# Kernel tuning notes

Measured on AMD Instinct MI355X. Metric: run time of the kernel, lower is better.

## Reference

```python
import jax, jax.numpy as jnp
import numpy as np

# MLS-MPM constants (init_kwargs)
N_GRID = 128
DT = 2e-4
DX = 1.0 / N_GRID
INV_DX = float(N_GRID)
P_VOL = (DX * 0.5) ** 3
P_RHO = 1000.0
P_MASS = P_VOL * P_RHO
GRAVITY = 9.8
BOUND = 3
N_PART = 500_000

# 27 neighbor offsets for quadratic B-spline stencil
_OFFS = np.stack(np.meshgrid(np.arange(3), np.arange(3), np.arange(3), indexing='ij'), -1).reshape(27, 3)


def setup_inputs() -> dict:
    key = jax.random.key(0)
    k1, k2, k3, k4, k5 = jax.random.split(key, 5)
    # particles strictly inside the domain, away from boundary cells
    x = 0.2 + 0.6 * jax.random.uniform(k1, (N_PART, 3), dtype=jnp.float32)
    v = 0.1 * jax.random.normal(k2, (N_PART, 3), dtype=jnp.float32)
    C = 0.1 * jax.random.normal(k3, (N_PART, 3, 3), dtype=jnp.float32)
    F = jnp.eye(3, dtype=jnp.float32) + 0.01 * jax.random.normal(k4, (N_PART, 3, 3), dtype=jnp.float32)
    stress = 1e2 * jax.random.normal(k5, (N_PART, 3, 3), dtype=jnp.float32)
    return {"x": x, "v": v, "C": C, "F": F, "stress": stress}


def _mpm_step(x, v, C, F, stress):
    dtype = x.dtype
    base = jnp.floor(x * INV_DX - 0.5).astype(jnp.int32)          # [N,3]
    fx = x * INV_DX - base.astype(dtype)                          # [N,3] in [0.5, 1.5)
    # quadratic B-spline weights per node offset (0,1,2) per axis: [N,3off,3ax]
    w = jnp.stack([0.5 * (1.5 - fx) ** 2,
                   0.75 - (fx - 1.0) ** 2,
                   0.5 * (fx - 0.5) ** 2], axis=1)
    offs = jnp.asarray(_OFFS, dtype=jnp.int32)                    # [27,3]
    weight = w[:, offs[:, 0], 0] * w[:, offs[:, 1], 1] * w[:, offs[:, 2], 2]  # [N,27]
    dpos = (offs[None].astype(dtype) - fx[:, None, :]) * DX       # [N,27,3] world units

    # P2G scatter: momentum (3) + mass (1) per grid node
    affine = (-DT * P_VOL * 4.0 * INV_DX * INV_DX) * stress + P_MASS * C   # [N,3,3]
    mv = P_MASS * v[:, None, :] + jnp.einsum('nij,nkj->nki', affine, dpos) # [N,27,3]
    vals = jnp.concatenate([weight[..., None] * mv,
                            (weight * P_MASS)[..., None]], axis=-1)        # [N,27,4]
    node = jnp.clip(base[:, None, :] + offs[None], 0, N_GRID - 1)          # [N,27,3]
    flat = (node[..., 0] * N_GRID + node[..., 1]) * N_GRID + node[..., 2]  # [N,27]
    grid = jnp.zeros((N_GRID ** 3, 4), dtype).at[flat.reshape(-1)].add(vals.reshape(-1, 4))

    # grid update: normalize momentum, gravity, sticky boundary
    gm = grid[:, 3:4]
    occ = gm[:, 0] > 0
    gv = jnp.where(gm > 0, grid[:, :3] / jnp.maximum(gm, 1e-10), 0.0)
    gv = gv.at[:, 1].add(jnp.where(occ, jnp.asarray(-DT * GRAVITY, dtype), 0.0))
    gv3 = gv.reshape(N_GRID, N_GRID, N_GRID, 3)
    idx = jnp.arange(N_GRID)
    for axis in range(3):  # fixed 3-axis loop (not a data loop)
        shp = [1, 1, 1]; shp[axis] = N_GRID
        lo = (idx < BOUND).reshape(shp)
        hi = (idx >= N_GRID - BOUND).reshape(shp)
        comp = gv3[..., axis]
        comp = jnp.where(lo & (comp < 0), 0.0, comp)
        comp = jnp.where(hi & (comp > 0), 0.0, comp)
        gv3 = gv3.at[..., axis].set(comp)
    gvf = gv3.reshape(-1, 3)

    # G2P gather
    gvp = gvf[flat]                                               # [N,27,3]
    v_next = jnp.einsum('nk,nkd->nd', weight, gvp)
    C_next = (4.0 * INV_DX * INV_DX) * jnp.einsum('nk,nki,nkj->nij', weight, gvp, dpos)
    x_next = x + DT * v_next
    F_next = jnp.einsum('nij,njk->nik', jnp.eye(3, dtype=dtype) + DT * C_next, F)
    return x_next, v_next, C_next, F_next


def reference(x, v, C, F, stress):
    return _mpm_step(x, v, C, F, stress)
```

## Files before the change

kernel.cpp:

```cpp
#include <hip/hip_runtime.h>
#include <limits.h>

#define N_GRID 128
#define N_GRID3 (N_GRID * N_GRID * N_GRID)

constexpr int   N_PART   = 500000;
constexpr float DT       = 0.0002f;
constexpr float DX       = 1.0f / 128.0f;
constexpr float INV_DX   = 128.0f;
constexpr float P_MASS   = 5.9604644775390625e-05f;
constexpr float AFF_COEF = -7.8125e-07f;
constexpr float GRAVITY  = 9.8f;
constexpr int   BOUND    = 3;
constexpr float C_SCALE  = 65536.0f;
constexpr int   ZQ       = 2;

__global__ __launch_bounds__(256) void k_count(const float* __restrict__ x,
                                               int* __restrict__ cnt,
                                               int* __restrict__ blkMin,
                                               int* __restrict__ blkMax) {
  __shared__ int lmin[12], lmax[12];
  int n = blockIdx.x * 256 + threadIdx.x;
  int bx = INT_MAX, by = INT_MAX, bz = INT_MAX;
  int mx = -1, my = -1, mz = -1;
  if (n < N_PART) {
    bx = min(max((int)floorf(x[n * 3 + 0] * INV_DX - 0.5f), 0), N_GRID - 1);
    by = min(max((int)floorf(x[n * 3 + 1] * INV_DX - 0.5f), 0), N_GRID - 1);
    bz = min(max((int)floorf(x[n * 3 + 2] * INV_DX - 0.5f), 0), N_GRID - 1);
    int c = (bx << 14) | (by << 7) | bz;
    atomicAdd(&cnt[c], 1);
    mx = bx; my = by; mz = bz;
  }
#pragma unroll
  for (int d = 32; d > 0; d >>= 1) {
    bx = min(bx, __shfl_xor(bx, d));
    by = min(by, __shfl_xor(by, d));
    bz = min(bz, __shfl_xor(bz, d));
    mx = max(mx, __shfl_xor(mx, d));
    my = max(my, __shfl_xor(my, d));
    mz = max(mz, __shfl_xor(mz, d));
  }
  int lane = threadIdx.x & 63, wid = threadIdx.x >> 6;
  if (lane == 0) {
    lmin[wid * 3 + 0] = bx; lmin[wid * 3 + 1] = by; lmin[wid * 3 + 2] = bz;
    lmax[wid * 3 + 0] = mx; lmax[wid * 3 + 1] = my; lmax[wid * 3 + 2] = mz;
  }
  __syncthreads();
  if (threadIdx.x == 0) {
    int b = blockIdx.x;
#pragma unroll
    for (int a = 0; a < 3; ++a) {
      blkMin[b * 3 + a] = min(min(lmin[a], lmin[3 + a]), min(lmin[6 + a], lmin[9 + a]));
      blkMax[b * 3 + a] = max(max(lmax[a], lmax[3 + a]), max(lmax[6 + a], lmax[9 + a]));
    }
  }
}

__global__ __launch_bounds__(256) void k_scan1(const int* __restrict__ cnt,
                                               int* __restrict__ blkSum) {
  __shared__ int ws[4];
  int tid = threadIdx.x, lane = tid & 63, wid = tid >> 6;
  int4 v = ((const int4*)cnt)[blockIdx.x * 256 + tid];
  int s = v.x + v.y + v.z + v.w;
  for (int d = 32; d > 0; d >>= 1) s += __shfl_down(s, d);
  if (lane == 0) ws[wid] = s;
  __syncthreads();
  if (tid == 0) blkSum[blockIdx.x] = ws[0] + ws[1] + ws[2] + ws[3];
}

__global__ __launch_bounds__(256) void k_scan2(const int* __restrict__ blkSum,
                                               int* __restrict__ blkOff,
                                               int* __restrict__ start,
                                               const int* __restrict__ blkMin,
                                               const int* __restrict__ blkMax,
                                               int nblkP,
                                               int* __restrict__ bbox) {
  __shared__ int wsum[4];
  __shared__ int rmin[12], rmax[12];
  int tid = threadIdx.x, lane = tid & 63, wid = tid >> 6;

  int base = tid * 8;
  int s[8], tot = 0;
#pragma unroll
  for (int j = 0; j < 8; ++j) { s[j] = blkSum[base + j]; tot += s[j]; }
  int incl = tot;
  for (int d = 1; d < 64; d <<= 1) {
    int t = __shfl_up(incl, d);
    if (lane >= d) incl += t;
  }
  if (lane == 63) wsum[wid] = incl;
  __syncthreads();
  int woff = 0;
  for (int w = 0; w < wid; ++w) woff += wsum[w];
  int run = woff + incl - tot;
#pragma unroll
  for (int j = 0; j < 8; ++j) { blkOff[base + j] = run; run += s[j]; }
  if (tid == 255) start[N_GRID3] = run;

  int bx = INT_MAX, by = INT_MAX, bz = INT_MAX;
  int mx = -1, my = -1, mz = -1;
  for (int j = tid; j < nblkP; j += 256) {
    bx = min(bx, blkMin[j * 3 + 0]);
    by = min(by, blkMin[j * 3 + 1]);
    bz = min(bz, blkMin[j * 3 + 2]);
    mx = max(mx, blkMax[j * 3 + 0]);
    my = max(my, blkMax[j * 3 + 1]);
    mz = max(mz, blkMax[j * 3 + 2]);
  }
#pragma unroll
  for (int d = 32; d > 0; d >>= 1) {
    bx = min(bx, __shfl_xor(bx, d));
    by = min(by, __shfl_xor(by, d));
    bz = min(bz, __shfl_xor(bz, d));
    mx = max(mx, __shfl_xor(mx, d));
    my = max(my, __shfl_xor(my, d));
    mz = max(mz, __shfl_xor(mz, d));
  }
  if (lane == 0) {
    rmin[wid * 3 + 0] = bx; rmin[wid * 3 + 1] = by; rmin[wid * 3 + 2] = bz;
    rmax[wid * 3 + 0] = mx; rmax[wid * 3 + 1] = my; rmax[wid * 3 + 2] = mz;
  }
  __syncthreads();
  if (tid == 0) {
#pragma unroll
    for (int a = 0; a < 3; ++a) {
      bbox[a]     = min(min(rmin[a], rmin[3 + a]), min(rmin[6 + a], rmin[9 + a]));
      bbox[3 + a] = max(max(rmax[a], rmax[3 + a]), max(rmax[6 + a], rmax[9 + a]));
    }
  }
}

__global__ __launch_bounds__(256) void k_scan3(int* __restrict__ cnt,
                                               const int* __restrict__ blkOff,
                                               int* __restrict__ start) {
  __shared__ int wsum[4];
  int tid = threadIdx.x, lane = tid & 63, wid = tid >> 6;
  int b = blockIdx.x;
  int4 v = ((const int4*)cnt)[b * 256 + tid];
  int s = v.x + v.y + v.z + v.w;
  int incl = s;
  for (int d = 1; d < 64; d <<= 1) {
    int t = __shfl_up(incl, d);
    if (lane >= d) incl += t;
  }
  if (lane == 63) wsum[wid] = incl;
  __syncthreads();
  int woff = blkOff[b];
  for (int w = 0; w < wid; ++w) woff += wsum[w];
  int run = woff + incl - s;
  int i0 = (b * 256 + tid) * 4;
  int r0 = run, r1 = r0 + v.x, r2 = r1 + v.y, r3 = r2 + v.z;
  start[i0 + 0] = r0; start[i0 + 1] = r1; start[i0 + 2] = r2; start[i0 + 3] = r3;
  cnt[i0 + 0] = r0; cnt[i0 + 1] = r1; cnt[i0 + 2] = r2; cnt[i0 + 3] = r3;
}

__global__ __launch_bounds__(256) void k_reorder(
    const float* __restrict__ x, const float* __restrict__ v,
    const float* __restrict__ C, const float* __restrict__ S,
    int* __restrict__ cursor, float4* __restrict__ posO,
    float4* __restrict__ aux) {
  int n = blockIdx.x * 256 + threadIdx.x;
  if (n >= N_PART) return;

  float px = x[n * 3 + 0], py = x[n * 3 + 1], pz = x[n * 3 + 2];
  int bx = min(max((int)floorf(px * INV_DX - 0.5f), 0), N_GRID - 1);
  int by = min(max((int)floorf(py * INV_DX - 0.5f), 0), N_GRID - 1);
  int bz = min(max((int)floorf(pz * INV_DX - 0.5f), 0), N_GRID - 1);
  int c = (bx << 14) | (by << 7) | bz;
  int pos = atomicAdd(&cursor[c], 1);

  float mvx = P_MASS * v[n * 3 + 0];
  float mvy = P_MASS * v[n * 3 + 1];
  float mvz = P_MASS * v[n * 3 + 2];
  float aff[9];
#pragma unroll
  for (int k = 0; k < 9; ++k)
    aff[k] = AFF_COEF * S[n * 9 + k] + P_MASS * C[n * 9 + k];

  posO[pos] = make_float4(px, py, pz, __int_as_float(n));
  float4* dst = aux + (size_t)pos * 3;
  dst[0] = make_float4(mvx, mvy, mvz, aff[0]);
  dst[1] = make_float4(aff[1], aff[2], aff[3], aff[4]);
  dst[2] = make_float4(aff[5], aff[6], aff[7], aff[8]);
}

__device__ __forceinline__ float wq(int o, float f) {
  if (o == 0) return 0.5f * (1.5f - f) * (1.5f - f);
  if (o == 1) return 0.75f - (f - 1.0f) * (f - 1.0f);
  return 0.5f * (f - 0.5f) * (f - 0.5f);
}

__global__ __launch_bounds__(256) void mpm_p2g(
    const int* __restrict__ start, const float4* __restrict__ posO,
    const float4* __restrict__ aux, const int* __restrict__ bbox,
    float* __restrict__ grid ) {
  int bx0 = bbox[0], by0 = bbox[1], bz0c = bbox[2];
  int nxd = bbox[3] - bx0 + 3;
  int nyd = bbox[4] - by0 + 3;
  int nzd = bbox[5] - bz0c + 3;
  int dimzq = (nzd + ZQ - 1) / ZQ;
  int vol = nxd * nyd * dimzq;
  int nact = (vol + 255) >> 8;

  int bid = blockIdx.x;
  if (bid >= nact) return;
  int q = nact >> 3, r = nact & 7;
  int xcd = bid & 7, sub = bid >> 3;
  int wgid = (xcd < r ? xcd * (q + 1) : r * (q + 1) + (xcd - r) * q) + sub;

  int t = wgid * 256 + (int)threadIdx.x;
  if (t >= vol) return;
  int izq = t % dimzq;
  int rr = t / dimzq;
  int iy = rr % nyd;
  int ix = rr / nyd;
  int nx = bx0 + ix, ny = by0 + iy, nz0 = bz0c + izq * ZQ;
  if (nx > N_GRID - 1 || ny > N_GRID - 1) return;
  int zb0 = nz0 - 2;
  bool zint = (zb0 >= 0) && (zb0 + ZQ + 2 <= N_GRID);

  float accx[ZQ], accy[ZQ], accz[ZQ], accm[ZQ];
#pragma unroll
  for (int k = 0; k < ZQ; ++k) { accx[k] = 0.f; accy[k] = 0.f; accz[k] = 0.f; accm[k] = 0.f; }
  int gotmask = 0;

#pragma unroll
  for (int dy = -2; dy <= 0; ++dy) {
    int cy = ny + dy;
    if (cy < 0) continue;
#pragma unroll
    for (int dx = -2; dx <= 0; ++dx) {
      int cx = nx + dx;
      if (cx < 0) continue;
      const int ox = -dx, oy = -dy;
      int rowb = (cx << 14) | (cy << 7);

      int S[ZQ + 3];
      if (zint) {
#pragma unroll
        for (int j = 0; j < ZQ + 3; ++j) S[j] = start[rowb + zb0 + j];
      } else {
#pragma unroll
        for (int j = 0; j < ZQ + 3; ++j)
          S[j] = start[rowb + min(max(zb0 + j, 0), N_GRID)];
      }
#pragma unroll
      for (int k = 0; k < ZQ; ++k)
        gotmask |= (S[k + 3] > S[k]) ? (1 << k) : 0;

      for (int i = S[0]; i < S[ZQ + 2]; ++i) {
        float4 q0 = posO[i];
        const float4* ap = aux + (size_t)i * 3;
        float4 A0 = ap[0], A1 = ap[1], A2 = ap[2];

        float fx = q0.x * INV_DX - (float)cx;
        float fy = q0.y * INV_DX - (float)cy;
        float gz = q0.z * INV_DX;
        float bzf = floorf(gz - 0.5f);
        float fz = gz - bzf;
        int oz0 = nz0 - (int)bzf;

        float wxy = wq(ox, fx) * wq(oy, fy);
        float dpx = ((float)ox - fx) * DX;
        float dpy = ((float)oy - fy) * DX;
        float wz0 = 0.5f * (1.5f - fz) * (1.5f - fz);
        float wz1 = 0.75f - (fz - 1.0f) * (fz - 1.0f);
        float wz2 = 0.5f * (fz - 0.5f) * (fz - 0.5f);

        float sx = A0.x + A0.w * dpx + A1.x * dpy;
        float sy = A0.y + A1.z * dpx + A1.w * dpy;
        float sz = A0.z + A2.y * dpx + A2.z * dpy;
        float wm = wxy * P_MASS;

#pragma unroll
        for (int k = 0; k < ZQ; ++k) {
          int oz = oz0 + k;
          if (oz < 0 || oz > 2) continue;
          float wzz = (oz == 0) ? wz0 : ((oz == 1) ? wz1 : wz2);
          float w = wxy * wzz;
          float dpz = ((float)oz - fz) * DX;
          accx[k] += w * (sx + A1.y * dpz);
          accy[k] += w * (sy + A2.x * dpz);
          accz[k] += w * (sz + A2.w * dpz);
          accm[k] += wzz * wm;
        }
      }
    }
  }

  if (!gotmask) return;

  float4* g4 = (float4*)grid;
#pragma unroll
  for (int k = 0; k < ZQ; ++k) {
    int nz = nz0 + k;
    if (!((gotmask >> k) & 1) || nz > N_GRID - 1) continue;
    float m = accm[k];
    float ovx = 0.0f, ovy = 0.0f, ovz = 0.0f;
    if (m > 0.0f) {
      float inv = 1.0f / fmaxf(m, 1e-10f);
      ovx = accx[k] * inv;
      ovy = accy[k] * inv;
      ovz = accz[k] * inv;
      ovy -= DT * GRAVITY;
    }
    if (nx < BOUND && ovx < 0.0f) ovx = 0.0f;
    if (nx >= N_GRID - BOUND && ovx > 0.0f) ovx = 0.0f;
    if (ny < BOUND && ovy < 0.0f) ovy = 0.0f;
    if (ny >= N_GRID - BOUND && ovy > 0.0f) ovy = 0.0f;
    if (nz < BOUND && ovz < 0.0f) ovz = 0.0f;
    if (nz >= N_GRID - BOUND && ovz > 0.0f) ovz = 0.0f;
    g4[(nx << 14) | (ny << 7) | nz] = make_float4(ovx, ovy, ovz, m);
  }
}

__global__ __launch_bounds__(256) void mpm_g2p(
    const float4* __restrict__ posO, const float* __restrict__ F,
    const float* __restrict__ grid,
    float* __restrict__ out_x, float* __restrict__ out_v,
    float* __restrict__ out_C, float* __restrict__ out_F) {
  int i = blockIdx.x * blockDim.x + threadIdx.x;
  if (i >= N_PART) return;

  float4 q0 = posO[i];
  int n = __float_as_int(q0.w);

  float px = q0.x, py = q0.y, pz = q0.z;
  float gx = px * INV_DX, gy = py * INV_DX, gz = pz * INV_DX;
  int bx = (int)floorf(gx - 0.5f);
  int by = (int)floorf(gy - 0.5f);
  int bz = (int)floorf(gz - 0.5f);
  float fx = gx - (float)bx, fy = gy - (float)by, fz = gz - (float)bz;

  float wx[3], wy[3], wz[3];
  wx[0] = 0.5f * (1.5f - fx) * (1.5f - fx);
  wx[1] = 0.75f - (fx - 1.0f) * (fx - 1.0f);
  wx[2] = 0.5f * (fx - 0.5f) * (fx - 0.5f);
  wy[0] = 0.5f * (1.5f - fy) * (1.5f - fy);
  wy[1] = 0.75f - (fy - 1.0f) * (fy - 1.0f);
  wy[2] = 0.5f * (fy - 0.5f) * (fy - 0.5f);
  wz[0] = 0.5f * (1.5f - fz) * (1.5f - fz);
  wz[1] = 0.75f - (fz - 1.0f) * (fz - 1.0f);
  wz[2] = 0.5f * (fz - 0.5f) * (fz - 0.5f);

  float vnx = 0.0f, vny = 0.0f, vnz = 0.0f;
  float Cn[9];
#pragma unroll
  for (int k = 0; k < 9; ++k) Cn[k] = 0.0f;

  const float4* g4 = (const float4*)grid;
  bool interior = (bx >= 0) & (by >= 0) & (bz >= 0) &
                  (bx + 2 < N_GRID) & (by + 2 < N_GRID) & (bz + 2 < N_GRID);

  if (interior) {
    int flat0 = (bx << 14) | (by << 7) | bz;
#pragma unroll
    for (int a = 0; a < 3; ++a) {
#pragma unroll
      for (int bb = 0; bb < 3; ++bb) {
#pragma unroll
        for (int c = 0; c < 3; ++c) {
          float weight = wx[a] * wy[bb] * wz[c];
          float dpx = ((float)a - fx) * DX;
          float dpy = ((float)bb - fy) * DX;
          float dpz = ((float)c - fz) * DX;
          float4 g = g4[flat0 + (a << 14) + (bb << 7) + c];
          vnx += weight * g.x;
          vny += weight * g.y;
          vnz += weight * g.z;
          Cn[0] += weight * g.x * dpx;
          Cn[1] += weight * g.x * dpy;
          Cn[2] += weight * g.x * dpz;
          Cn[3] += weight * g.y * dpx;
          Cn[4] += weight * g.y * dpy;
          Cn[5] += weight * g.y * dpz;
          Cn[6] += weight * g.z * dpx;
          Cn[7] += weight * g.z * dpy;
          Cn[8] += weight * g.z * dpz;
        }
      }
    }
  } else {
#pragma unroll
    for (int a = 0; a < 3; ++a) {
#pragma unroll
      for (int bb = 0; bb < 3; ++bb) {
#pragma unroll
        for (int c = 0; c < 3; ++c) {
          float weight = wx[a] * wy[bb] * wz[c];
          float dpx = ((float)a - fx) * DX;
          float dpy = ((float)bb - fy) * DX;
          float dpz = ((float)c - fz) * DX;
          int nxg = min(max(bx + a, 0), N_GRID - 1);
          int nyg = min(max(by + bb, 0), N_GRID - 1);
          int nzg = min(max(bz + c, 0), N_GRID - 1);
          float4 g = g4[(nxg << 14) | (nyg << 7) | nzg];
          vnx += weight * g.x;
          vny += weight * g.y;
          vnz += weight * g.z;
          Cn[0] += weight * g.x * dpx;
          Cn[1] += weight * g.x * dpy;
          Cn[2] += weight * g.x * dpz;
          Cn[3] += weight * g.y * dpx;
          Cn[4] += weight * g.y * dpy;
          Cn[5] += weight * g.y * dpz;
          Cn[6] += weight * g.z * dpx;
          Cn[7] += weight * g.z * dpy;
          Cn[8] += weight * g.z * dpz;
        }
      }
    }
  }

#pragma unroll
  for (int k = 0; k < 9; ++k) Cn[k] *= C_SCALE;

  out_x[n * 3 + 0] = px + DT * vnx;
  out_x[n * 3 + 1] = py + DT * vny;
  out_x[n * 3 + 2] = pz + DT * vnz;
  out_v[n * 3 + 0] = vnx;
  out_v[n * 3 + 1] = vny;
  out_v[n * 3 + 2] = vnz;

  float A[9];
#pragma unroll
  for (int k = 0; k < 9; ++k) A[k] = DT * Cn[k];
  A[0] += 1.0f; A[4] += 1.0f; A[8] += 1.0f;

  float Fl[9];
#pragma unroll
  for (int k = 0; k < 9; ++k) Fl[k] = F[n * 9 + k];

#pragma unroll
  for (int r = 0; r < 3; ++r) {
#pragma unroll
    for (int k = 0; k < 3; ++k) {
      float s = A[r * 3 + 0] * Fl[0 * 3 + k] +
                A[r * 3 + 1] * Fl[1 * 3 + k] +
                A[r * 3 + 2] * Fl[2 * 3 + k];
      out_F[n * 9 + r * 3 + k] = s;
    }
  }

#pragma unroll
  for (int k = 0; k < 9; ++k) out_C[n * 9 + k] = Cn[k];
}

extern "C" void kernel_launch(void* const* d_in, const int* in_sizes, int n_in,
                              void* d_out, int out_size, void* d_ws, size_t ws_size,
                              hipStream_t stream) {
  const float* x      = (const float*)d_in[0];
  const float* v      = (const float*)d_in[1];
  const float* C      = (const float*)d_in[2];
  const float* F      = (const float*)d_in[3];
  const float* stress = (const float*)d_in[4];

  float* out = (float*)d_out;
  char*  ws  = (char*)d_ws;

  const size_t GRID_BYTES  = (size_t)N_GRID3 * 4 * sizeof(float);
  const size_t POSO_BYTES  = (size_t)N_PART * sizeof(float4);
  const size_t AUX_BYTES   = (size_t)N_PART * 3 * sizeof(float4);
  const size_t CNT_BYTES   = (size_t)N_GRID3 * sizeof(int);
  const size_t START_BYTES = ((size_t)N_GRID3 + 1) * sizeof(int);

  int pblocks = (N_PART + 255) / 256;

  float*  grid   = (float*)ws;
  float4* posO   = (float4*)(ws + GRID_BYTES);
  float4* aux    = (float4*)(ws + GRID_BYTES + POSO_BYTES);
  int*    cnt    = (int*)(ws + GRID_BYTES + POSO_BYTES + AUX_BYTES);
  int*    startp = (int*)(ws + GRID_BYTES + POSO_BYTES + AUX_BYTES + CNT_BYTES);
  int*    blkSum = (int*)(ws + GRID_BYTES + POSO_BYTES + AUX_BYTES + CNT_BYTES + START_BYTES);
  int*    blkOff = blkSum + 2048;
  int*    blkMin = blkOff + 2048;
  int*    blkMax = blkMin + pblocks * 3;
  int*    bbox   = blkMax + pblocks * 3;

  hipMemsetAsync(cnt, 0, CNT_BYTES, stream);

  k_count<<<pblocks, 256, 0, stream>>>(x, cnt, blkMin, blkMax);
  k_scan1<<<2048, 256, 0, stream>>>(cnt, blkSum);
  k_scan2<<<1, 256, 0, stream>>>(blkSum, blkOff, startp, blkMin, blkMax, pblocks, bbox);
  k_scan3<<<2048, 256, 0, stream>>>(cnt, blkOff, startp);
  k_reorder<<<pblocks, 256, 0, stream>>>(x, v, C, stress, cnt, posO, aux);

  mpm_p2g<<<(N_GRID3 / ZQ + 255) / 256, 256, 0, stream>>>(startp, posO, aux, bbox, grid);

  float* out_x = out;
  float* out_v = out + (size_t)N_PART * 3;
  float* out_C = out + (size_t)N_PART * 6;
  float* out_F = out + (size_t)N_PART * 6 + (size_t)N_PART * 9;
  mpm_g2p<<<pblocks, 256, 0, stream>>>(posO, F, grid, out_x, out_v, out_C, out_F);
}
```

Before: 204.9 us.

## Tile P2G gather into 8x8x4 node bricks with particles staged in LDS

The per-thread gather P2G, where each thread read particles from global memory for its two z-nodes, becomes a brick-based kernel. Each 256-thread workgroup owns an 8x8x4 node brick and computes the cell column prefix sums of its halo region. It cooperatively copies all contributing particles (position plus affine data) into shared memory, and each thread then accumulates its node from LDS, cutting repeated global and L2 reads of the same particle by neighbouring nodes. Bricks whose halo holds more than 896 particles fall back to the direct global-memory path. The shared-memory footprint (~58KB) limits occupancy, and the per-particle binary search and extra barriers add overhead.

```diff
diff --git a/kernel.cpp b/kernel.cpp
--- a/kernel.cpp
+++ b/kernel.cpp
@@ -13,7 +13,13 @@
 constexpr float GRAVITY  = 9.8f;
 constexpr int   BOUND    = 3;
 constexpr float C_SCALE  = 65536.0f;
-constexpr int   ZQ       = 2;
+
+constexpr int BBX = 8, BBY = 8, BBZ = 4;
+constexpr int RX = BBX + 2, RY = BBY + 2;
+constexpr int NCOL = RX * RY;
+constexpr int RZB = BBZ + 3;
+constexpr int CAP = 896;
+constexpr int MAX_BRICKS = 17 * 17 * 33;
 
 __global__ __launch_bounds__(256) void k_count(const float* __restrict__ x,
                                                int* __restrict__ cnt,
@@ -194,124 +200,206 @@
     const int* __restrict__ start, const float4* __restrict__ posO,
     const float4* __restrict__ aux, const int* __restrict__ bbox,
     float* __restrict__ grid ) {
+  __shared__ float4 ldsPos[CAP];
+  __shared__ float4 ldsA0[CAP];
+  __shared__ float4 ldsA1[CAP];
+  __shared__ float4 ldsA2[CAP];
+  __shared__ int    ldsBnd[NCOL * RZB];
+  __shared__ int    colSrc[NCOL];
+  __shared__ int    colPre[NCOL + 1];
+  __shared__ int    s_w0tot;
+
   int bx0 = bbox[0], by0 = bbox[1], bz0c = bbox[2];
-  int nxd = bbox[3] - bx0 + 3;
-  int nyd = bbox[4] - by0 + 3;
-  int nzd = bbox[5] - bz0c + 3;
-  int dimzq = (nzd + ZQ - 1) / ZQ;
-  int vol = nxd * nyd * dimzq;
-  int nact = (vol + 255) >> 8;
-
+  int nxd = bbox[3] - bx0 + 3, nyd = bbox[4] - by0 + 3, nzd = bbox[5] - bz0c + 3;
+  int nbx = (nxd + BBX - 1) / BBX;
+  int nby = (nyd + BBY - 1) / BBY;
+  int nbz = (nzd + BBZ - 1) / BBZ;
+  int nact = nbx * nby * nbz;
   int bid = blockIdx.x;
   if (bid >= nact) return;
   int q = nact >> 3, r = nact & 7;
   int xcd = bid & 7, sub = bid >> 3;
-  int wgid = (xcd < r ? xcd * (q + 1) : r * (q + 1) + (xcd - r) * q) + sub;
-
-  int t = wgid * 256 + (int)threadIdx.x;
-  if (t >= vol) return;
-  int izq = t % dimzq;
-  int rr = t / dimzq;
-  int iy = rr % nyd;
-  int ix = rr / nyd;
-  int nx = bx0 + ix, ny = by0 + iy, nz0 = bz0c + izq * ZQ;
-  if (nx > N_GRID - 1 || ny > N_GRID - 1) return;
-  int zb0 = nz0 - 2;
-  bool zint = (zb0 >= 0) && (zb0 + ZQ + 2 <= N_GRID);
-
-  float accx[ZQ], accy[ZQ], accz[ZQ], accm[ZQ];
-#pragma unroll
-  for (int k = 0; k < ZQ; ++k) { accx[k] = 0.f; accy[k] = 0.f; accz[k] = 0.f; accm[k] = 0.f; }
-  int gotmask = 0;
-
-#pragma unroll
-  for (int dy = -2; dy <= 0; ++dy) {
-    int cy = ny + dy;
-    if (cy < 0) continue;
-#pragma unroll
-    for (int dx = -2; dx <= 0; ++dx) {
-      int cx = nx + dx;
-      if (cx < 0) continue;
-      const int ox = -dx, oy = -dy;
-      int rowb = (cx << 14) | (cy << 7);
-
-      int S[ZQ + 3];
-      if (zint) {
-#pragma unroll
-        for (int j = 0; j < ZQ + 3; ++j) S[j] = start[rowb + zb0 + j];
-      } else {
-#pragma unroll
-        for (int j = 0; j < ZQ + 3; ++j)
-          S[j] = start[rowb + min(max(zb0 + j, 0), N_GRID)];
+  int wg = (xcd < r ? xcd * (q + 1) : r * (q + 1) + (xcd - r) * q) + sub;
+  int bzi = wg % nbz; int tt = wg / nbz; int byi = tt % nby; int bxi = tt / nby;
+  int ox = bx0 + bxi * BBX, oy = by0 + byi * BBY, oz = bz0c + bzi * BBZ;
+
+  int tid = threadIdx.x;
+
+  int cnt_t = 0;
+  if (tid < NCOL) {
+    int rcx = tid / RY, rcy = tid % RY;
+    int sx = ox - 2 + rcx, sy = oy - 2 + rcy;
+    int b[RZB];
+    if (sx >= 0 && sx < N_GRID && sy >= 0 && sy < N_GRID) {
+      int rowb = (sx << 14) | (sy << 7);
+      int zl0 = oz - 2;
+#pragma unroll
+      for (int j = 0; j < RZB; ++j)
+        b[j] = start[rowb + min(max(zl0 + j, 0), N_GRID)];
+    } else {
+#pragma unroll
+      for (int j = 0; j < RZB; ++j) b[j] = 0;
+    }
+    colSrc[tid] = b[0];
+#pragma unroll
+    for (int j = 0; j < RZB; ++j) ldsBnd[tid * RZB + j] = b[j] - b[0];
+    cnt_t = b[RZB - 1] - b[0];
+  }
+  int excl = 0;
+  if (tid < 128) {
+    int lane = tid & 63;
+    int incl = cnt_t;
+#pragma unroll
+    for (int d = 1; d < 64; d <<= 1) {
+      int tv = __shfl_up(incl, d);
+      if (lane >= d) incl += tv;
+    }
+    excl = incl - cnt_t;
+    if (tid == 63) s_w0tot = incl;
+  }
+  __syncthreads();
+  if (tid < 128) {
+    int off = (tid >= 64) ? s_w0tot : 0;
+    if (tid < NCOL) colPre[tid] = excl + off;
+    if (tid == 127) colPre[NCOL] = excl + off;
+  }
+  __syncthreads();
+  int T = colPre[NCOL];
+  if (T == 0) return;
+  bool overflow = (T > CAP);
+
+  if (!overflow) {
+    if (tid < NCOL) {
+      int p0 = colPre[tid];
+#pragma unroll
+      for (int j = 0; j < RZB; ++j) ldsBnd[tid * RZB + j] += p0;
+    }
+    __syncthreads();
+    for (int p = tid; p < T; p += 256) {
+      int lo = 0, hi = NCOL;
+      while (hi - lo > 1) {
+        int mid = (lo + hi) >> 1;
+        if (colPre[mid] <= p) lo = mid; else hi = mid;
       }
-#pragma unroll
-      for (int k = 0; k < ZQ; ++k)
-        gotmask |= (S[k + 3] > S[k]) ? (1 << k) : 0;
-
-      for (int i = S[0]; i < S[ZQ + 2]; ++i) {
-        float4 q0 = posO[i];
-        const float4* ap = aux + (size_t)i * 3;
-        float4 A0 = ap[0], A1 = ap[1], A2 = ap[2];
-
-        float fx = q0.x * INV_DX - (float)cx;
-        float fy = q0.y * INV_DX - (float)cy;
-        float gz = q0.z * INV_DX;
-        float bzf = floorf(gz - 0.5f);
-        float fz = gz - bzf;
-        int oz0 = nz0 - (int)bzf;
-
-        float wxy = wq(ox, fx) * wq(oy, fy);
-        float dpx = ((float)ox - fx) * DX;
-        float dpy = ((float)oy - fy) * DX;
-        float wz0 = 0.5f * (1.5f - fz) * (1.5f - fz);
-        float wz1 = 0.75f - (fz - 1.0f) * (fz - 1.0f);
-        float wz2 = 0.5f * (fz - 0.5f) * (fz - 0.5f);
-
-        float sx = A0.x + A0.w * dpx + A1.x * dpy;
-        float sy = A0.y + A1.z * dpx + A1.w * dpy;
-        float sz = A0.z + A2.y * dpx + A2.z * dpy;
-        float wm = wxy * P_MASS;
-
-#pragma unroll
-        for (int k = 0; k < ZQ; ++k) {
-          int oz = oz0 + k;
-          if (oz < 0 || oz > 2) continue;
-          float wzz = (oz == 0) ? wz0 : ((oz == 1) ? wz1 : wz2);
+      int src = colSrc[lo] + (p - colPre[lo]);
+      ldsPos[p] = posO[src];
+      const float4* ap = aux + (size_t)src * 3;
+      ldsA0[p] = ap[0]; ldsA1[p] = ap[1]; ldsA2[p] = ap[2];
+    }
+    __syncthreads();
+  }
+
+  int lz = tid & 3, ly = (tid >> 2) & 7, lx = tid >> 5;
+  int nx = ox + lx, ny = oy + ly, nz = oz + lz;
+  bool inrange = (nx < N_GRID) && (ny < N_GRID) && (nz < N_GRID);
+
+  float accx = 0.f, accy = 0.f, accz = 0.f, accm = 0.f;
+  int got = 0;
+
+  if (!overflow) {
+#pragma unroll
+    for (int dy = 0; dy < 3; ++dy) {
+#pragma unroll
+      for (int dx = 0; dx < 3; ++dx) {
+        const int oxw = 2 - dx, oyw = 2 - dy;
+        int rc = (lx + dx) * RY + (ly + dy);
+        int s = ldsBnd[rc * RZB + lz];
+        int e = ldsBnd[rc * RZB + lz + 3];
+        got |= (e - s);
+        float sxf = (float)(ox - 2 + lx + dx);
+        float syf = (float)(oy - 2 + ly + dy);
+        for (int p = s; p < e; ++p) {
+          float4 q0 = ldsPos[p];
+          float4 A0 = ldsA0[p], A1 = ldsA1[p], A2 = ldsA2[p];
+          float fx = q0.x * INV_DX - sxf;
+          float fy = q0.y * INV_DX - syf;
+          float gz = q0.z * INV_DX;
+          float bzf = floorf(gz - 0.5f);
+          float fz = gz - bzf;
+          int ozw = nz - (int)bzf;
+          if (ozw < 0 || ozw > 2) continue;
+          float wxy = wq(oxw, fx) * wq(oyw, fy);
+          float dpx = ((float)oxw - fx) * DX;
+          float dpy = ((float)oyw - fy) * DX;
+          float wzz = (ozw == 0) ? (0.5f * (1.5f - fz) * (1.5f - fz))
+                    : ((ozw == 1) ? (0.75f - (fz - 1.0f) * (fz - 1.0f))
+                                  : (0.5f * (fz - 0.5f) * (fz - 0.5f)));
           float w = wxy * wzz;
-          float dpz = ((float)oz - fz) * DX;
-          accx[k] += w * (sx + A1.y * dpz);
-          accy[k] += w * (sy + A2.x * dpz);
-          accz[k] += w * (sz + A2.w * dpz);
-          accm[k] += wzz * wm;
+          float dpz = ((float)ozw - fz) * DX;
+          float sx_ = A0.x + A0.w * dpx + A1.x * dpy;
+          float sy_ = A0.y + A1.z * dpx + A1.w * dpy;
+          float sz_ = A0.z + A2.y * dpx + A2.z * dpy;
+          accx += w * (sx_ + A1.y * dpz);
+          accy += w * (sy_ + A2.x * dpz);
+          accz += w * (sz_ + A2.w * dpz);
+          accm += wzz * wxy * P_MASS;
         }
       }
     }
-  }
-
-  if (!gotmask) return;
-
-  float4* g4 = (float4*)grid;
-#pragma unroll
-  for (int k = 0; k < ZQ; ++k) {
-    int nz = nz0 + k;
-    if (!((gotmask >> k) & 1) || nz > N_GRID - 1) continue;
-    float m = accm[k];
-    float ovx = 0.0f, ovy = 0.0f, ovz = 0.0f;
-    if (m > 0.0f) {
-      float inv = 1.0f / fmaxf(m, 1e-10f);
-      ovx = accx[k] * inv;
-      ovy = accy[k] * inv;
-      ovz = accz[k] * inv;
-      ovy -= DT * GRAVITY;
-    }
-    if (nx < BOUND && ovx < 0.0f) ovx = 0.0f;
-    if (nx >= N_GRID - BOUND && ovx > 0.0f) ovx = 0.0f;
-    if (ny < BOUND && ovy < 0.0f) ovy = 0.0f;
-    if (ny >= N_GRID - BOUND && ovy > 0.0f) ovy = 0.0f;
-    if (nz < BOUND && ovz < 0.0f) ovz = 0.0f;
-    if (nz >= N_GRID - BOUND && ovz > 0.0f) ovz = 0.0f;
-    g4[(nx << 14) | (ny << 7) | nz] = make_float4(ovx, ovy, ovz, m);
-  }
+  } else {
+#pragma unroll
+    for (int dy = 0; dy < 3; ++dy) {
+      int sy = ny + dy - 2;
+      if (sy < 0 || sy >= N_GRID) continue;
+#pragma unroll
+      for (int dx = 0; dx < 3; ++dx) {
+        int sx = nx + dx - 2;
+        if (sx < 0 || sx >= N_GRID) continue;
+        const int oxw = 2 - dx, oyw = 2 - dy;
+        int rowb = (sx << 14) | (sy << 7);
+        int s = start[rowb + max(nz - 2, 0)];
+        int e = start[rowb + min(nz + 1, N_GRID)];
+        got |= (e - s);
+        float sxf = (float)sx, syf = (float)sy;
+        for (int i = s; i < e; ++i) {
+          float4 q0 = posO[i];
+          const float4* ap = aux + (size_t)i * 3;
+          float4 A0 = ap[0], A1 = ap[1], A2 = ap[2];
+          float fx = q0.x * INV_DX - sxf;
+          float fy = q0.y * INV_DX - syf;
+          float gz = q0.z * INV_DX;
+          float bzf = floorf(gz - 0.5f);
+          float fz = gz - bzf;
+          int ozw = nz - (int)bzf;
+          if (ozw < 0 || ozw > 2) continue;
+          float wxy = wq(oxw, fx) * wq(oyw, fy);
+          float dpx = ((float)oxw - fx) * DX;
+          float dpy = ((float)oyw - fy) * DX;
+          float wzz = (ozw == 0) ? (0.5f * (1.5f - fz) * (1.5f - fz))
+                    : ((ozw == 1) ? (0.75f - (fz - 1.0f) * (fz - 1.0f))
+                                  : (0.5f * (fz - 0.5f) * (fz - 0.5f)));
+          float w = wxy * wzz;
+          float dpz = ((float)ozw - fz) * DX;
+          float sx_ = A0.x + A0.w * dpx + A1.x * dpy;
+          float sy_ = A0.y + A1.z * dpx + A1.w * dpy;
+          float sz_ = A0.z + A2.y * dpx + A2.z * dpy;
+          accx += w * (sx_ + A1.y * dpz);
+          accy += w * (sy_ + A2.x * dpz);
+          accz += w * (sz_ + A2.w * dpz);
+          accm += wzz * wxy * P_MASS;
+        }
+      }
+    }
+  }
+
+  if (!got || !inrange) return;
+
+  float m = accm;
+  float ovx = 0.0f, ovy = 0.0f, ovz = 0.0f;
+  if (m > 0.0f) {
+    float inv = 1.0f / fmaxf(m, 1e-10f);
+    ovx = accx * inv;
+    ovy = accy * inv;
+    ovz = accz * inv;
+    ovy -= DT * GRAVITY;
+  }
+  if (nx < BOUND && ovx < 0.0f) ovx = 0.0f;
+  if (nx >= N_GRID - BOUND && ovx > 0.0f) ovx = 0.0f;
+  if (ny < BOUND && ovy < 0.0f) ovy = 0.0f;
+  if (ny >= N_GRID - BOUND && ovy > 0.0f) ovy = 0.0f;
+  if (nz < BOUND && ovz < 0.0f) ovz = 0.0f;
+  if (nz >= N_GRID - BOUND && ovz > 0.0f) ovz = 0.0f;
+  ((float4*)grid)[(nx << 14) | (ny << 7) | nz] = make_float4(ovx, ovy, ovz, m);
 }
 
 __global__ __launch_bounds__(256) void mpm_g2p(
@@ -485,7 +573,7 @@
   k_scan3<<<2048, 256, 0, stream>>>(cnt, blkOff, startp);
   k_reorder<<<pblocks, 256, 0, stream>>>(x, v, C, stress, cnt, posO, aux);
 
-  mpm_p2g<<<(N_GRID3 / ZQ + 255) / 256, 256, 0, stream>>>(startp, posO, aux, bbox, grid);
+  mpm_p2g<<<MAX_BRICKS, 256, 0, stream>>>(startp, posO, aux, bbox, grid);
 
   float* out_x = out;
   float* out_v = out + (size_t)N_PART * 3;
```

Measured after the change: 229.8 us. +12.2%, slower.
